# Kernel tuning notes

Measured on AMD Instinct MI355X. Metric: run time of the kernel, lower is better.

The kernel has to match this reference:

```python
import jax, jax.numpy as jnp
import numpy as np

EMBED_DIM = 512
NUM_HEADS = 8
HEAD_DIM = EMBED_DIM // NUM_HEADS


def setup_inputs() -> dict:
    key = jax.random.key(0)
    k1, k2, k3, k4, k5, k6 = jax.random.split(key, 6)
    B, S, D = 2, 4096, EMBED_DIM
    scale = 1.0 / np.sqrt(D)
    return {
        "inputs": jax.random.normal(k1, (B, S, D), dtype=jnp.float32),
        "Wq": jax.random.normal(k2, (D, D), dtype=jnp.float32) * scale,
        "Wk": jax.random.normal(k3, (D, D), dtype=jnp.float32) * scale,
        "Wv": jax.random.normal(k4, (D, D), dtype=jnp.float32) * scale,
        "Wc": jax.random.normal(k5, (D, D), dtype=jnp.float32) * scale,
        "bc": jax.random.normal(k6, (D,), dtype=jnp.float32) * 0.01,
    }


def reference(inputs, Wq, Wk, Wv, Wc, bc):
    B, S, D = inputs.shape
    H, Hd = NUM_HEADS, HEAD_DIM

    def split_heads(x):
        # [B,S,D] -> [B,H,S,Hd]
        return x.reshape(B, S, H, Hd).transpose(0, 2, 1, 3)

    # nn.Linear applies x @ W.T
    q = split_heads(inputs @ Wq.T).astype(jnp.float32)
    k = split_heads(inputs @ Wk.T).astype(jnp.float32)
    v = split_heads(inputs @ Wv.T).astype(jnp.float32)

    scores = jnp.einsum("bhqd,bhkd->bhqk", q, k) / np.sqrt(Hd).astype(jnp.float32)
    weights = jax.nn.softmax(scores, axis=-1)
    attended = jnp.einsum("bhqk,bhkd->bhqd", weights, v).astype(inputs.dtype)
    attended = attended.transpose(0, 2, 1, 3).reshape(B, S, D)
    return attended @ Wc.T + bc
```

## Files before the change

### kernel.cpp

```cpp
#include <hip/hip_runtime.h>
#include <cstdint>
#include <cstddef>

typedef _Float16 half_t;
typedef half_t h8 __attribute__((ext_vector_type(8)));
typedef half_t h4 __attribute__((ext_vector_type(4)));
typedef float f4 __attribute__((ext_vector_type(4)));
typedef unsigned int u32;

static constexpr int S_LEN  = 4096;
static constexpr int DMODEL = 512;
static constexpr int NH     = 8;
static constexpr int HD     = 64;
static constexpr int BATCH  = 2;
static constexpr int MTOK   = BATCH * S_LEN;

#define QSCALE 0.18033688011112043f

__device__ __forceinline__ void g2lds16(const void* g, void* l) {
    __builtin_amdgcn_global_load_lds(
        (const __attribute__((address_space(1))) u32*)(uintptr_t)g,
        (__attribute__((address_space(3))) u32*)(u32)(uintptr_t)l,
        16, 0, 0);
}

__device__ __forceinline__ f4 mfma16(h8 a, h8 b, f4 c) {
    return __builtin_amdgcn_mfma_f32_16x16x32_f16(a, b, c, 0, 0, 0);
}

__global__ void cvt_x(const float* __restrict__ in, half_t* __restrict__ out) {
    int i = (blockIdx.x * 256 + threadIdx.x) * 8;
    const float4* p = (const float4*)(in + i);
    float4 a = p[0], b = p[1];
    h8 h;
    h[0]=(half_t)a.x; h[1]=(half_t)a.y; h[2]=(half_t)a.z; h[3]=(half_t)a.w;
    h[4]=(half_t)b.x; h[5]=(half_t)b.y; h[6]=(half_t)b.z; h[7]=(half_t)b.w;
    *(h8*)(out + i) = h;
}

__global__ void cvt_w(const float* __restrict__ w0, const float* __restrict__ w1,
                      const float* __restrict__ w2, const float* __restrict__ w3,
                      half_t* __restrict__ o0, half_t* __restrict__ o1,
                      half_t* __restrict__ o2, half_t* __restrict__ o3) {
    int y = blockIdx.y;
    const float* in = (y==0) ? w0 : (y==1) ? w1 : (y==2) ? w2 : w3;
    half_t* out     = (y==0) ? o0 : (y==1) ? o1 : (y==2) ? o2 : o3;
    float s = (y==0) ? QSCALE : 1.0f;
    int i = (blockIdx.x * 256 + threadIdx.x) * 8;
    const float4* p = (const float4*)(in + i);
    float4 a = p[0], b = p[1];
    h8 h;
    h[0]=(half_t)(a.x*s); h[1]=(half_t)(a.y*s); h[2]=(half_t)(a.z*s); h[3]=(half_t)(a.w*s);
    h[4]=(half_t)(b.x*s); h[5]=(half_t)(b.y*s); h[6]=(half_t)(b.z*s); h[7]=(half_t)(b.w*s);
    *(h8*)(out + i) = h;
}

__device__ __forceinline__ void gemm_core2(const half_t* __restrict__ A,
                                           const half_t* __restrict__ B,
                                           int m0, int n0, int Kdim,
                                           half_t* As, half_t* Bs,
                                           f4 (&acc)[2][4]) {
    const int tid  = threadIdx.x;
    const int lane = tid & 63;
    const int w    = tid >> 6;
    const int quad = lane >> 4;
    const int low  = lane & 15;
    const int wr   = (w >> 1) * 32;
    const int wc   = (w & 1) * 64;

    f4 zero = {0.f, 0.f, 0.f, 0.f};
    #pragma unroll
    for (int i = 0; i < 2; ++i)
        #pragma unroll
        for (int j = 0; j < 4; ++j) acc[i][j] = zero;

    for (int kk = 0; kk < Kdim; kk += 32) {
        __syncthreads();
        {
            int c = tid;
            int row = c >> 2, cs = c & 3;
            int gc = cs ^ ((row >> 1) & 3);
            g2lds16(A + (size_t)(m0 + row) * Kdim + kk + gc * 8, As + c * 8);
        }
        #pragma unroll
        for (int it = 0; it < 2; ++it) {
            int c = tid + 256 * it;
            int row = c >> 2, cs = c & 3;
            int gc = cs ^ ((row >> 1) & 3);
            g2lds16(B + (size_t)(n0 + row) * Kdim + kk + gc * 8, Bs + c * 8);
        }
        __syncthreads();

        h8 af[2], bf[4];
        #pragma unroll
        for (int i = 0; i < 2; ++i) {
            int r = wr + i * 16 + low;
            af[i] = *(const h8*)(As + r * 32 + (quad ^ ((r >> 1) & 3)) * 8);
        }
        #pragma unroll
        for (int j = 0; j < 4; ++j) {
            int r = wc + j * 16 + low;
            bf[j] = *(const h8*)(Bs + r * 32 + (quad ^ ((r >> 1) & 3)) * 8);
        }
        #pragma unroll
        for (int i = 0; i < 2; ++i)
            #pragma unroll
            for (int j = 0; j < 4; ++j)
                acc[i][j] = mfma16(af[i], bf[j], acc[i][j]);
    }
}

__global__ __launch_bounds__(256, 4) void gemm_proj(
    const half_t* __restrict__ X,
    const half_t* __restrict__ Wq, const half_t* __restrict__ Wk, const half_t* __restrict__ Wv,
    half_t* __restrict__ Q, half_t* __restrict__ K, half_t* __restrict__ Vt) {
    __shared__ half_t As[64 * 32];
    __shared__ half_t Bs[128 * 32];
    const int z  = blockIdx.z;
    const int bx = blockIdx.x;

    const half_t *A, *B;
    int m0, n0;
    if (z < 2) {
        A = X; B = (z == 0) ? Wq : Wk;
        m0 = (bx >> 2) * 64; n0 = (bx & 3) * 128;
    } else {
        A = Wv; B = X;
        m0 = (bx & 7) * 64; n0 = (bx >> 3) * 128;
    }
    f4 acc[2][4];
    gemm_core2(A, B, m0, n0, DMODEL, As, Bs, acc);

    const int lane = threadIdx.x & 63;
    const int w    = threadIdx.x >> 6;
    const int quad = lane >> 4, low = lane & 15;
    const int wr = (w >> 1) * 32, wc = (w & 1) * 64;

    if (z < 2) {
        half_t* O = (z == 0) ? Q : K;
        #pragma unroll
        for (int i = 0; i < 2; ++i) {
            int mb = m0 + wr + i * 16 + quad * 4;
            #pragma unroll
            for (int j = 0; j < 4; ++j) {
                int n = n0 + wc + j * 16 + low;
                int h = n >> 6, d = n & 63;
                #pragma unroll
                for (int r = 0; r < 4; ++r) {
                    int m = mb + r;
                    int b = m >> 12, s = m & 4095;
                    size_t idx = (((size_t)(b * NH + h) << 12) + s) * 64 + d;
                    O[idx] = (half_t)acc[i][j][r];
                }
            }
        }
    } else {
        #pragma unroll
        for (int i = 0; i < 2; ++i) {
            int dgb = m0 + wr + i * 16 + quad * 4;
            #pragma unroll
            for (int j = 0; j < 4; ++j) {
                int tok = n0 + wc + j * 16 + low;
                int b = tok >> 12, s = tok & 4095;
                #pragma unroll
                for (int r = 0; r < 4; ++r) {
                    int dg = dgb + r;
                    size_t idx = (((size_t)(b * NH + (dg >> 6)) << 18)) + ((dg & 63) << 12) + s;
                    Vt[idx] = (half_t)acc[i][j][r];
                }
            }
        }
    }
}

__global__ __launch_bounds__(256, 4) void gemm_out(
    const half_t* __restrict__ A, const half_t* __restrict__ W,
    const float* __restrict__ bias, float* __restrict__ out) {
    __shared__ half_t As[64 * 32];
    __shared__ half_t Bs[128 * 32];
    const int bx = blockIdx.x;
    const int m0 = (bx >> 2) * 64;
    const int n0 = (bx & 3) * 128;
    f4 acc[2][4];
    gemm_core2(A, W, m0, n0, DMODEL, As, Bs, acc);

    const int lane = threadIdx.x & 63;
    const int w    = threadIdx.x >> 6;
    const int quad = lane >> 4, low = lane & 15;
    const int wr = (w >> 1) * 32, wc = (w & 1) * 64;

    #pragma unroll
    for (int i = 0; i < 2; ++i) {
        int mb = m0 + wr + i * 16 + quad * 4;
        #pragma unroll
        for (int j = 0; j < 4; ++j) {
            int n = n0 + wc + j * 16 + low;
            float bv = bias[n];
            #pragma unroll
            for (int r = 0; r < 4; ++r)
                out[(size_t)(mb + r) * DMODEL + n] = acc[i][j][r] + bv;
        }
    }
}

__global__ __launch_bounds__(256, 2) void flash_attn(
    const half_t* __restrict__ Q,
    const half_t* __restrict__ K,
    const half_t* __restrict__ V,
    half_t* __restrict__ Oa) {
    __shared__ half_t Ks[2][128 * 64];
    __shared__ half_t Vs[2][64 * 128];
    __shared__ half_t Ps[2][4 * 32 * 32];

    const int tid  = threadIdx.x;
    const int lane = tid & 63;
    const int w    = tid >> 6;
    const int quad = lane >> 4, low = lane & 15;
    const int bh = blockIdx.y;
    const int q0 = blockIdx.x * 128 + w * 32;

    const half_t* Qb = Q + ((size_t)bh << 18);
    const half_t* Kb = K + ((size_t)bh << 18);
    const half_t* Vb = V + ((size_t)bh << 18);

    h8 qf[2][2];
    #pragma unroll
    for (int i = 0; i < 2; ++i)
        #pragma unroll
        for (int ks = 0; ks < 2; ++ks)
            qf[i][ks] = *(const h8*)(Qb + (size_t)(q0 + i * 16 + low) * 64 + ks * 32 + quad * 8);

    f4 Oacc[2][4];
    f4 zero = {0.f, 0.f, 0.f, 0.f};
    #pragma unroll
    for (int i = 0; i < 2; ++i)
        #pragma unroll
        for (int j = 0; j < 4; ++j) Oacc[i][j] = zero;
    float lrun[2] = {0.f, 0.f};

    auto stage = [&](int k0, int p) {
        #pragma unroll
        for (int it = 0; it < 4; ++it) {
            int c = tid + 256 * it;
            int key = c >> 3, cs = c & 7;
            int gc = cs ^ (key & 7);
            g2lds16(Kb + (size_t)(k0 + key) * 64 + gc * 8, &Ks[p][c * 8]);
        }
        #pragma unroll
        for (int it = 0; it < 4; ++it) {
            int c = tid + 256 * it;
            int d = c >> 4, cs = c & 15;
            int gc = cs ^ (d & 7);
            g2lds16(Vb + (size_t)d * S_LEN + k0 + gc * 8, &Vs[p][c * 8]);
        }
    };

    stage(0, 0);

    for (int c = 0; c < S_LEN / 128; ++c) {
        __syncthreads();
        if (c + 1 < S_LEN / 128) stage((c + 1) * 128, (c + 1) & 1);

        const half_t* Kc = Ks[c & 1];
        const half_t* Vc = Vs[c & 1];

        f4 sc[2][8];
        #pragma unroll
        for (int nt = 0; nt < 8; ++nt) {
            int key = nt * 16 + low;
            h8 kf0 = *(const h8*)(Kc + key * 64 + ((0 + quad) ^ (key & 7)) * 8);
            h8 kf1 = *(const h8*)(Kc + key * 64 + ((4 + quad) ^ (key & 7)) * 8);
            #pragma unroll
            for (int i = 0; i < 2; ++i) {
                sc[i][nt] = mfma16(kf0, qf[i][0], zero);
                sc[i][nt] = mfma16(kf1, qf[i][1], sc[i][nt]);
            }
        }

        #pragma unroll
        for (int i = 0; i < 2; ++i) {
            float rs = 0.f;
            #pragma unroll
            for (int nt = 0; nt < 8; ++nt)
                #pragma unroll
                for (int r = 0; r < 4; ++r) {
                    float p = __builtin_amdgcn_exp2f(sc[i][nt][r]);
                    sc[i][nt][r] = p;
                    rs += p;
                }
            lrun[i] += rs;
        }

        #pragma unroll
        for (int g = 0; g < 4; ++g) {
            half_t* Pw = &Ps[g & 1][w * (32 * 32)];
            #pragma unroll
            for (int i = 0; i < 2; ++i) {
                int q = i * 16 + low;
                #pragma unroll
                for (int hn = 0; hn < 2; ++hn) {
                    int nt = 2 * g + hn;
                    h4 pk;
                    pk[0] = (half_t)sc[i][nt][0];
                    pk[1] = (half_t)sc[i][nt][1];
                    pk[2] = (half_t)sc[i][nt][2];
                    pk[3] = (half_t)sc[i][nt][3];
                    int cc = (hn * 2 + (quad >> 1)) ^ ((q >> 1) & 3);
                    *(h4*)(Pw + q * 32 + cc * 8 + (quad & 1) * 4) = pk;
                }
            }
            h8 vf[4];
            #pragma unroll
            for (int j = 0; j < 4; ++j) {
                int d = j * 16 + low;
                vf[j] = *(const h8*)(Vc + d * 128 + (((g * 4 + quad)) ^ (d & 7)) * 8);
            }
            h8 pf[2];
            #pragma unroll
            for (int i = 0; i < 2; ++i) {
                int q = i * 16 + low;
                pf[i] = *(const h8*)(Pw + q * 32 + (quad ^ ((q >> 1) & 3)) * 8);
            }
            #pragma unroll
            for (int i = 0; i < 2; ++i)
                #pragma unroll
                for (int j = 0; j < 4; ++j)
                    Oacc[i][j] = mfma16(vf[j], pf[i], Oacc[i][j]);
        }
    }

    #pragma unroll
    for (int i = 0; i < 2; ++i) {
        lrun[i] += __shfl_xor(lrun[i], 16);
        lrun[i] += __shfl_xor(lrun[i], 32);
    }

    const int b = bh >> 3, h = bh & 7;
    #pragma unroll
    for (int i = 0; i < 2; ++i) {
        float inv = 1.0f / lrun[i];
        int qg = q0 + i * 16 + low;
        #pragma unroll
        for (int j = 0; j < 4; ++j) {
            h4 o;
            #pragma unroll
            for (int r = 0; r < 4; ++r) o[r] = (half_t)(Oacc[i][j][r] * inv);
            *(h4*)(Oa + ((size_t)(b * S_LEN + qg)) * DMODEL + h * 64 + j * 16 + quad * 4) = o;
        }
    }
}

extern "C" void kernel_launch(void* const* d_in, const int* in_sizes, int n_in,
                              void* d_out, int out_size, void* d_ws, size_t ws_size,
                              hipStream_t stream) {
    const float* X  = (const float*)d_in[0];
    const float* Wq = (const float*)d_in[1];
    const float* Wk = (const float*)d_in[2];
    const float* Wv = (const float*)d_in[3];
    const float* Wc = (const float*)d_in[4];
    const float* bc = (const float*)d_in[5];
    float* out = (float*)d_out;

    char* ws = (char*)d_ws;
    const size_t SZ_X = (size_t)MTOK * DMODEL * 2;
    const size_t SZ_W = (size_t)DMODEL * DMODEL * 2;
    half_t* Xh   = (half_t*)(ws);
    half_t* Wqh  = (half_t*)(ws + SZ_X);
    half_t* Wkh  = (half_t*)(ws + SZ_X + SZ_W);
    half_t* Wvh  = (half_t*)(ws + SZ_X + 2 * SZ_W);
    half_t* Wch  = (half_t*)(ws + SZ_X + 3 * SZ_W);
    half_t* Qh   = (half_t*)(ws + SZ_X + 4 * SZ_W);
    half_t* Kh   = (half_t*)(ws + 2 * SZ_X + 4 * SZ_W);
    half_t* Vt   = (half_t*)(ws + 3 * SZ_X + 4 * SZ_W);
    half_t* Att  = (half_t*)(ws + 4 * SZ_X + 4 * SZ_W);

    cvt_x<<<2048, 256, 0, stream>>>(X, Xh);
    cvt_w<<<dim3(128, 4), 256, 0, stream>>>(Wq, Wk, Wv, Wc, Wqh, Wkh, Wvh, Wch);
    gemm_proj<<<dim3(512, 1, 3), 256, 0, stream>>>(Xh, Wqh, Wkh, Wvh, Qh, Kh, Vt);
    flash_attn<<<dim3(32, 16), 256, 0, stream>>>(Qh, Kh, Vt, Att);
    gemm_out<<<512, 256, 0, stream>>>(Att, Wch, bc, out);
}
```

Measured before the change: 204.8 us.

## Load K/V fragments directly from global into registers, dropping LDS staging

Replaces the shared-memory double-buffered K/V tiles (loaded with global_load_lds) with per-wave direct global loads of K and V fragments into registers, prefetched one 32-key group ahead. This removes block-wide __syncthreads and the LDS round-trip, and frees LDS so more blocks could fit per CU. The cost is that each of the 4 waves now fetches the same K/V data separately from global/L2 (4x redundant traffic), with smaller per-iteration work and fewer memory ops in flight per load.

```diff
diff --git a/kernel.cpp b/kernel.cpp
--- a/kernel.cpp
+++ b/kernel.cpp
@@ -208,8 +208,6 @@
     const half_t* __restrict__ K,
     const half_t* __restrict__ V,
     half_t* __restrict__ Oa) {
-    __shared__ half_t Ks[2][128 * 64];
-    __shared__ half_t Vs[2][64 * 128];
     __shared__ half_t Ps[2][4 * 32 * 32];
 
     const int tid  = threadIdx.x;
@@ -238,95 +236,71 @@
         for (int j = 0; j < 4; ++j) Oacc[i][j] = zero;
     float lrun[2] = {0.f, 0.f};
 
-    auto stage = [&](int k0, int p) {
-        #pragma unroll
-        for (int it = 0; it < 4; ++it) {
-            int c = tid + 256 * it;
-            int key = c >> 3, cs = c & 7;
-            int gc = cs ^ (key & 7);
-            g2lds16(Kb + (size_t)(k0 + key) * 64 + gc * 8, &Ks[p][c * 8]);
-        }
-        #pragma unroll
-        for (int it = 0; it < 4; ++it) {
-            int c = tid + 256 * it;
-            int d = c >> 4, cs = c & 15;
-            int gc = cs ^ (d & 7);
-            g2lds16(Vb + (size_t)d * S_LEN + k0 + gc * 8, &Vs[p][c * 8]);
-        }
+    auto load_group = [&](int kw, h8 (&kf)[2][2], h8 (&vf)[4]) {
+        #pragma unroll
+        for (int nt = 0; nt < 2; ++nt)
+            #pragma unroll
+            for (int ks = 0; ks < 2; ++ks)
+                kf[nt][ks] = *(const h8*)(Kb + (size_t)(kw + nt * 16 + low) * 64 + ks * 32 + quad * 8);
+        #pragma unroll
+        for (int j = 0; j < 4; ++j)
+            vf[j] = *(const h8*)(Vb + (size_t)(j * 16 + low) * S_LEN + kw + quad * 8);
     };
 
-    stage(0, 0);
-
-    for (int c = 0; c < S_LEN / 128; ++c) {
-        __syncthreads();
-        if (c + 1 < S_LEN / 128) stage((c + 1) * 128, (c + 1) & 1);
-
-        const half_t* Kc = Ks[c & 1];
-        const half_t* Vc = Vs[c & 1];
-
-        f4 sc[2][8];
-        #pragma unroll
-        for (int nt = 0; nt < 8; ++nt) {
-            int key = nt * 16 + low;
-            h8 kf0 = *(const h8*)(Kc + key * 64 + ((0 + quad) ^ (key & 7)) * 8);
-            h8 kf1 = *(const h8*)(Kc + key * 64 + ((4 + quad) ^ (key & 7)) * 8);
+    constexpr int NG = S_LEN / 32;
+    h8 kfA[2][2], vfA[4];
+    load_group(0, kfA, vfA);
+
+    for (int gi = 0; gi < NG; ++gi) {
+        h8 kfB[2][2], vfB[4];
+        if (gi + 1 < NG) load_group((gi + 1) * 32, kfB, vfB);
+
+        f4 sc[2][2];
+        #pragma unroll
+        for (int hn = 0; hn < 2; ++hn)
             #pragma unroll
             for (int i = 0; i < 2; ++i) {
-                sc[i][nt] = mfma16(kf0, qf[i][0], zero);
-                sc[i][nt] = mfma16(kf1, qf[i][1], sc[i][nt]);
+                sc[i][hn] = mfma16(kfA[hn][0], qf[i][0], zero);
+                sc[i][hn] = mfma16(kfA[hn][1], qf[i][1], sc[i][hn]);
             }
-        }
-
-        #pragma unroll
-        for (int i = 0; i < 2; ++i) {
-            float rs = 0.f;
-            #pragma unroll
-            for (int nt = 0; nt < 8; ++nt)
-                #pragma unroll
-                for (int r = 0; r < 4; ++r) {
-                    float p = __builtin_amdgcn_exp2f(sc[i][nt][r]);
-                    sc[i][nt][r] = p;
-                    rs += p;
-                }
-            lrun[i] += rs;
-        }
-
-        #pragma unroll
-        for (int g = 0; g < 4; ++g) {
-            half_t* Pw = &Ps[g & 1][w * (32 * 32)];
-            #pragma unroll
-            for (int i = 0; i < 2; ++i) {
-                int q = i * 16 + low;
-                #pragma unroll
-                for (int hn = 0; hn < 2; ++hn) {
-                    int nt = 2 * g + hn;
-                    h4 pk;
-                    pk[0] = (half_t)sc[i][nt][0];
-                    pk[1] = (half_t)sc[i][nt][1];
-                    pk[2] = (half_t)sc[i][nt][2];
-                    pk[3] = (half_t)sc[i][nt][3];
-                    int cc = (hn * 2 + (quad >> 1)) ^ ((q >> 1) & 3);
-                    *(h4*)(Pw + q * 32 + cc * 8 + (quad & 1) * 4) = pk;
-                }
+
+        half_t* Pw = &Ps[gi & 1][w * (32 * 32)];
+        #pragma unroll
+        for (int i = 0; i < 2; ++i) {
+            int q = i * 16 + low;
+            #pragma unroll
+            for (int hn = 0; hn < 2; ++hn) {
+                float p0 = __builtin_amdgcn_exp2f(sc[i][hn][0]);
+                float p1 = __builtin_amdgcn_exp2f(sc[i][hn][1]);
+                float p2 = __builtin_amdgcn_exp2f(sc[i][hn][2]);
+                float p3 = __builtin_amdgcn_exp2f(sc[i][hn][3]);
+                lrun[i] += (p0 + p1) + (p2 + p3);
+                h4 pk;
+                pk[0] = (half_t)p0; pk[1] = (half_t)p1;
+                pk[2] = (half_t)p2; pk[3] = (half_t)p3;
+                int cc = (hn * 2 + (quad >> 1)) ^ ((q >> 1) & 3);
+                *(h4*)(Pw + q * 32 + cc * 8 + (quad & 1) * 4) = pk;
             }
-            h8 vf[4];
-            #pragma unroll
-            for (int j = 0; j < 4; ++j) {
-                int d = j * 16 + low;
-                vf[j] = *(const h8*)(Vc + d * 128 + (((g * 4 + quad)) ^ (d & 7)) * 8);
-            }
-            h8 pf[2];
-            #pragma unroll
-            for (int i = 0; i < 2; ++i) {
-                int q = i * 16 + low;
-                pf[i] = *(const h8*)(Pw + q * 32 + (quad ^ ((q >> 1) & 3)) * 8);
-            }
-            #pragma unroll
-            for (int i = 0; i < 2; ++i)
-                #pragma unroll
-                for (int j = 0; j < 4; ++j)
-                    Oacc[i][j] = mfma16(vf[j], pf[i], Oacc[i][j]);
-        }
+        }
+
+        h8 pf[2];
+        #pragma unroll
+        for (int i = 0; i < 2; ++i) {
+            int q = i * 16 + low;
+            pf[i] = *(const h8*)(Pw + q * 32 + (quad ^ ((q >> 1) & 3)) * 8);
+        }
+        #pragma unroll
+        for (int i = 0; i < 2; ++i)
+            #pragma unroll
+            for (int j = 0; j < 4; ++j)
+                Oacc[i][j] = mfma16(vfA[j], pf[i], Oacc[i][j]);
+
+        #pragma unroll
+        for (int nt = 0; nt < 2; ++nt)
+            #pragma unroll
+            for (int ks = 0; ks < 2; ++ks) kfA[nt][ks] = kfB[nt][ks];
+        #pragma unroll
+        for (int j = 0; j < 4; ++j) vfA[j] = vfB[j];
     }
 
     #pragma unroll
```

Result: slower. 348.4 us (+70.1%).

## Split attention keys across two blocks and merge partials in combine kernel

Applied to the files above, without the earlier changes.

Flash attention now splits the key sequence into two halves via blockIdx.z, doubling the grid from 512 to 1024 blocks. Each half writes unnormalized fp16 partial outputs and row sums, and a new combine kernel adds them and normalizes. The attention kernel drops LDS double-buffering and raises launch bounds to 4 blocks per CU, trading copy/compute overlap for occupancy. The two convert kernels are merged into one launch, and workspace buffers are reused. The cost is an extra kernel launch plus a round trip of partial outputs through memory.

```diff
diff --git a/kernel.cpp b/kernel.cpp
--- a/kernel.cpp
+++ b/kernel.cpp
@@ -28,25 +28,27 @@
     return __builtin_amdgcn_mfma_f32_16x16x32_f16(a, b, c, 0, 0, 0);
 }
 
-__global__ void cvt_x(const float* __restrict__ in, half_t* __restrict__ out) {
-    int i = (blockIdx.x * 256 + threadIdx.x) * 8;
-    const float4* p = (const float4*)(in + i);
-    float4 a = p[0], b = p[1];
-    h8 h;
-    h[0]=(half_t)a.x; h[1]=(half_t)a.y; h[2]=(half_t)a.z; h[3]=(half_t)a.w;
-    h[4]=(half_t)b.x; h[5]=(half_t)b.y; h[6]=(half_t)b.z; h[7]=(half_t)b.w;
-    *(h8*)(out + i) = h;
-}
-
-__global__ void cvt_w(const float* __restrict__ w0, const float* __restrict__ w1,
-                      const float* __restrict__ w2, const float* __restrict__ w3,
-                      half_t* __restrict__ o0, half_t* __restrict__ o1,
-                      half_t* __restrict__ o2, half_t* __restrict__ o3) {
-    int y = blockIdx.y;
-    const float* in = (y==0) ? w0 : (y==1) ? w1 : (y==2) ? w2 : w3;
-    half_t* out     = (y==0) ? o0 : (y==1) ? o1 : (y==2) ? o2 : o3;
-    float s = (y==0) ? QSCALE : 1.0f;
-    int i = (blockIdx.x * 256 + threadIdx.x) * 8;
+__global__ void cvt_all(const float* __restrict__ X,
+                        const float* __restrict__ w0, const float* __restrict__ w1,
+                        const float* __restrict__ w2, const float* __restrict__ w3,
+                        half_t* __restrict__ Xh,
+                        half_t* __restrict__ o0, half_t* __restrict__ o1,
+                        half_t* __restrict__ o2, half_t* __restrict__ o3) {
+    int bx = blockIdx.x;
+    const float* in;
+    half_t* out;
+    float s = 1.0f;
+    int i;
+    if (bx < 2048) {
+        in = X; out = Xh;
+        i = (bx * 256 + threadIdx.x) * 8;
+    } else {
+        int y = (bx - 2048) >> 7;
+        in  = (y==0) ? w0 : (y==1) ? w1 : (y==2) ? w2 : w3;
+        out = (y==0) ? o0 : (y==1) ? o1 : (y==2) ? o2 : o3;
+        if (y == 0) s = QSCALE;
+        i = (((bx - 2048) & 127) * 256 + threadIdx.x) * 8;
+    }
     const float4* p = (const float4*)(in + i);
     float4 a = p[0], b = p[1];
     h8 h;
@@ -203,25 +205,30 @@
     }
 }
 
-__global__ __launch_bounds__(256, 2) void flash_attn(
+__global__ __launch_bounds__(256, 4) void flash_attn(
     const half_t* __restrict__ Q,
     const half_t* __restrict__ K,
     const half_t* __restrict__ V,
-    half_t* __restrict__ Oa) {
-    __shared__ half_t Ks[2][128 * 64];
-    __shared__ half_t Vs[2][64 * 128];
-    __shared__ half_t Ps[2][4 * 32 * 32];
+    half_t* __restrict__ Oa0,
+    half_t* __restrict__ Oa1,
+    float*  __restrict__ Ls) {
+    __shared__ half_t Ks[128 * 64];
+    __shared__ half_t Vs[64 * 128];
+    __shared__ half_t Ps[4 * 32 * 32];
 
     const int tid  = threadIdx.x;
     const int lane = tid & 63;
     const int w    = tid >> 6;
     const int quad = lane >> 4, low = lane & 15;
     const int bh = blockIdx.y;
+    const int g  = blockIdx.z;
     const int q0 = blockIdx.x * 128 + w * 32;
+    const int kbase = g * (S_LEN / 2);
 
     const half_t* Qb = Q + ((size_t)bh << 18);
     const half_t* Kb = K + ((size_t)bh << 18);
     const half_t* Vb = V + ((size_t)bh << 18);
+    half_t* Oa = g ? Oa1 : Oa0;
 
     h8 qf[2][2];
     #pragma unroll
@@ -238,38 +245,33 @@
         for (int j = 0; j < 4; ++j) Oacc[i][j] = zero;
     float lrun[2] = {0.f, 0.f};
 
-    auto stage = [&](int k0, int p) {
+    half_t* Pw = Ps + w * (32 * 32);
+
+    for (int c = 0; c < S_LEN / 2 / 128; ++c) {
+        const int k0 = kbase + c * 128;
+        __syncthreads();
         #pragma unroll
         for (int it = 0; it < 4; ++it) {
-            int c = tid + 256 * it;
-            int key = c >> 3, cs = c & 7;
+            int cc = tid + 256 * it;
+            int key = cc >> 3, cs = cc & 7;
             int gc = cs ^ (key & 7);
-            g2lds16(Kb + (size_t)(k0 + key) * 64 + gc * 8, &Ks[p][c * 8]);
+            g2lds16(Kb + (size_t)(k0 + key) * 64 + gc * 8, Ks + cc * 8);
         }
         #pragma unroll
         for (int it = 0; it < 4; ++it) {
-            int c = tid + 256 * it;
-            int d = c >> 4, cs = c & 15;
+            int cc = tid + 256 * it;
+            int d = cc >> 4, cs = cc & 15;
             int gc = cs ^ (d & 7);
-            g2lds16(Vb + (size_t)d * S_LEN + k0 + gc * 8, &Vs[p][c * 8]);
-        }
-    };
-
-    stage(0, 0);
-
-    for (int c = 0; c < S_LEN / 128; ++c) {
+            g2lds16(Vb + (size_t)d * S_LEN + k0 + gc * 8, Vs + cc * 8);
+        }
         __syncthreads();
-        if (c + 1 < S_LEN / 128) stage((c + 1) * 128, (c + 1) & 1);
-
-        const half_t* Kc = Ks[c & 1];
-        const half_t* Vc = Vs[c & 1];
 
         f4 sc[2][8];
         #pragma unroll
         for (int nt = 0; nt < 8; ++nt) {
             int key = nt * 16 + low;
-            h8 kf0 = *(const h8*)(Kc + key * 64 + ((0 + quad) ^ (key & 7)) * 8);
-            h8 kf1 = *(const h8*)(Kc + key * 64 + ((4 + quad) ^ (key & 7)) * 8);
+            h8 kf0 = *(const h8*)(Ks + key * 64 + ((0 + quad) ^ (key & 7)) * 8);
+            h8 kf1 = *(const h8*)(Ks + key * 64 + ((4 + quad) ^ (key & 7)) * 8);
             #pragma unroll
             for (int i = 0; i < 2; ++i) {
                 sc[i][nt] = mfma16(kf0, qf[i][0], zero);
@@ -292,14 +294,13 @@
         }
 
         #pragma unroll
-        for (int g = 0; g < 4; ++g) {
-            half_t* Pw = &Ps[g & 1][w * (32 * 32)];
+        for (int gg = 0; gg < 4; ++gg) {
             #pragma unroll
             for (int i = 0; i < 2; ++i) {
                 int q = i * 16 + low;
                 #pragma unroll
                 for (int hn = 0; hn < 2; ++hn) {
-                    int nt = 2 * g + hn;
+                    int nt = 2 * gg + hn;
                     h4 pk;
                     pk[0] = (half_t)sc[i][nt][0];
                     pk[1] = (half_t)sc[i][nt][1];
@@ -313,7 +314,7 @@
             #pragma unroll
             for (int j = 0; j < 4; ++j) {
                 int d = j * 16 + low;
-                vf[j] = *(const h8*)(Vc + d * 128 + (((g * 4 + quad)) ^ (d & 7)) * 8);
+                vf[j] = *(const h8*)(Vs + d * 128 + (((gg * 4 + quad)) ^ (d & 7)) * 8);
             }
             h8 pf[2];
             #pragma unroll
@@ -338,16 +339,36 @@
     const int b = bh >> 3, h = bh & 7;
     #pragma unroll
     for (int i = 0; i < 2; ++i) {
-        float inv = 1.0f / lrun[i];
         int qg = q0 + i * 16 + low;
+        if (quad == 0)
+            Ls[(((size_t)g * 16 + bh) << 12) + qg] = lrun[i];
         #pragma unroll
         for (int j = 0; j < 4; ++j) {
             h4 o;
             #pragma unroll
-            for (int r = 0; r < 4; ++r) o[r] = (half_t)(Oacc[i][j][r] * inv);
+            for (int r = 0; r < 4; ++r) o[r] = (half_t)Oacc[i][j][r];
             *(h4*)(Oa + ((size_t)(b * S_LEN + qg)) * DMODEL + h * 64 + j * 16 + quad * 4) = o;
         }
     }
+}
+
+__global__ void combine(const half_t* __restrict__ O0, const half_t* __restrict__ O1,
+                        const float* __restrict__ Ls, half_t* __restrict__ Att) {
+    int i = blockIdx.x * 256 + threadIdx.x;
+    int idx = i * 8;
+    int tok = idx >> 9;
+    int col = idx & 511;
+    int b = tok >> 12, s = tok & 4095, h = col >> 6;
+    int bh = b * NH + h;
+    float l = Ls[((size_t)bh << 12) + s] + Ls[(((size_t)16 + bh) << 12) + s];
+    float inv = 1.0f / l;
+    h8 a = *(const h8*)(O0 + idx);
+    h8 c = *(const h8*)(O1 + idx);
+    h8 o;
+    #pragma unroll
+    for (int r = 0; r < 8; ++r)
+        o[r] = (half_t)(((float)a[r] + (float)c[r]) * inv);
+    *(h8*)(Att + idx) = o;
 }
 
 extern "C" void kernel_launch(void* const* d_in, const int* in_sizes, int n_in,
@@ -372,11 +393,14 @@
     half_t* Qh   = (half_t*)(ws + SZ_X + 4 * SZ_W);
     half_t* Kh   = (half_t*)(ws + 2 * SZ_X + 4 * SZ_W);
     half_t* Vt   = (half_t*)(ws + 3 * SZ_X + 4 * SZ_W);
-    half_t* Att  = (half_t*)(ws + 4 * SZ_X + 4 * SZ_W);
-
-    cvt_x<<<2048, 256, 0, stream>>>(X, Xh);
-    cvt_w<<<dim3(128, 4), 256, 0, stream>>>(Wq, Wk, Wv, Wc, Wqh, Wkh, Wvh, Wch);
+    half_t* Oa0  = (half_t*)(ws + 4 * SZ_X + 4 * SZ_W);
+    float*  Ls   = (float*) (ws + 5 * SZ_X + 4 * SZ_W);
+    half_t* Oa1  = Xh;
+    half_t* Att  = Qh;
+
+    cvt_all<<<2048 + 512, 256, 0, stream>>>(X, Wq, Wk, Wv, Wc, Xh, Wqh, Wkh, Wvh, Wch);
     gemm_proj<<<dim3(512, 1, 3), 256, 0, stream>>>(Xh, Wqh, Wkh, Wvh, Qh, Kh, Vt);
-    flash_attn<<<dim3(32, 16), 256, 0, stream>>>(Qh, Kh, Vt, Att);
+    flash_attn<<<dim3(32, 16, 2), 256, 0, stream>>>(Qh, Kh, Vt, Oa0, Oa1, Ls);
+    combine<<<2048, 256, 0, stream>>>(Oa0, Oa1, Ls, Att);
     gemm_out<<<512, 256, 0, stream>>>(Att, Wch, bc, out);
 }
```

Result: slower. 420.3 us (+105.2%).
